# Performance work log

Measured on AMD Instinct MI355X. Metric: run time of the kernel, lower is better.

## Reference

```python
import jax, jax.numpy as jnp
import numpy as np

N_HEADS = 4
N_HIDDEN = 64  # out_features (concat=False)
MASK_FILL = -9e15
ADJ_THRESH = 0.05


def setup_inputs() -> dict:
    key = jax.random.key(0)
    k1, k2, k3, k4 = jax.random.split(key, 4)
    B, S, N, F = 32, 20, 128, 64
    h = jax.random.normal(k1, (B, S, N, F), dtype=jnp.float32)
    adj_mat = jax.random.uniform(k2, (B, S, N, N), dtype=jnp.float32)
    W = jax.random.normal(k3, (F, N_HEADS * N_HIDDEN), dtype=jnp.float32) * (1.0 / np.sqrt(F))
    a = jax.random.normal(k4, (N_HEADS, 2 * N_HIDDEN, 1), dtype=jnp.float32) * 0.1
    return {"h": h, "adj_mat": adj_mat, "W": W, "a": a}


def reference(h, adj_mat, W, a):
    B, S, N, _ = h.shape
    # Linear projection (no bias); dropout is a no-op (training=False)
    ht = jnp.einsum('bsnf,fo->bsno', h, W)
    # (B, S, H, N, D)
    ht = ht.reshape(B, S, N, N_HEADS, N_HIDDEN).transpose(0, 1, 3, 2, 4)
    a_src = a[:, :N_HIDDEN, 0]   # (H, D)
    a_tgt = a[:, N_HIDDEN:, 0]   # (H, D)
    src = jnp.einsum('bshnd,hd->bshn', ht, a_src)  # (B,S,H,N)
    tgt = jnp.einsum('bshnd,hd->bshn', ht, a_tgt)
    # additive sigmoid score: e_ij = sigmoid(src_i + tgt_j)
    e = jax.nn.sigmoid(src[..., :, None] + tgt[..., None, :])  # (B,S,H,N,N)
    mask = (adj_mat < ADJ_THRESH)[:, :, None, :, :]  # broadcast over heads
    e = jnp.where(mask, MASK_FILL, e)
    attn = jax.nn.softmax(e, axis=-1)
    h_prime = jnp.einsum('bshij,bshjd->bshid', attn, ht)
    # concat=False -> mean over heads
    return h_prime.mean(axis=2)  # (B,S,N,D)
```

## Files before the change

kernel.cpp:

```cpp
#include <hip/hip_runtime.h>
#include <hip/hip_bf16.h>

#define ADJ_TH 0.05f

typedef __bf16 bf16x8 __attribute__((ext_vector_type(8)));
typedef __bf16 bf16x4 __attribute__((ext_vector_type(4)));
typedef float  f32x4  __attribute__((ext_vector_type(4)));

__global__ __launch_bounds__(256)
void prep_kernel(const float* __restrict__ W, const float* __restrict__ a,
                 __bf16* __restrict__ Wt, __bf16* __restrict__ WAt) {
    const int t = threadIdx.x;
    if (blockIdx.x == 0) {
        #pragma unroll 4
        for (int r = 0; r < 64; ++r) {
            int id = r * 256 + t;
            Wt[(id & 255) * 64 + (id >> 8)] = (__bf16)W[id];
        }
    } else {
        for (int id = t; id < 1024; id += 256) {
            int n = id >> 6, f = id & 63;
            float s = 0.f;
            if (n < 8) {
                int hh = n >> 1, st = n & 1;
                #pragma unroll 8
                for (int d = 0; d < 64; ++d)
                    s += W[f * 256 + hh * 64 + d] * a[hh * 128 + st * 64 + d];
            }
            WAt[n * 64 + f] = (__bf16)s;
        }
    }
}

__device__ __forceinline__ int sw_idx(int o, int i) {
    return o * 128 + ((((i >> 3) ^ o) & 15) << 3) + (i & 7);
}

__global__ __launch_bounds__(256, 3)
void gat_main_kernel(const float* __restrict__ hg, const float* __restrict__ adj,
                     const __bf16* __restrict__ Wt, const __bf16* __restrict__ WAt,
                     float* __restrict__ out)
{
    const int bs  = blockIdx.x;
    const int tid = threadIdx.x;
    const int w   = tid >> 6;
    const int l   = tid & 63;
    const int l15 = l & 15;
    const int l4  = l >> 4;

    __shared__ __bf16   ht_t[128 * 128];
    __shared__ float    src_sh[4][128];
    __shared__ float    tgt_sh[4][128];
    __shared__ unsigned mask_sh[512];

    const float* hb = hg  + (size_t)bs * 8192;
    const float* ab = adj + (size_t)bs * 16384;

    #pragma unroll 8
    for (int it = 0; it < 64; ++it) {
        int row = 32 * w + (it >> 1);
        int col = ((it & 1) << 6) + l;
        unsigned long long bal = __ballot(ab[row * 128 + col] < ADJ_TH);
        if (l < 2) mask_sh[row * 4 + ((it & 1) << 1) + l] = (unsigned)(bal >> (32 * l));
    }

    bf16x8 af[2][2];
    #pragma unroll
    for (int m2 = 0; m2 < 2; ++m2) {
        int row = 16 * (2 * w + m2) + l15;
        #pragma unroll
        for (int ks = 0; ks < 2; ++ks) {
            const float4* p4 = reinterpret_cast<const float4*>(hb + row * 64 + 8 * l4 + 32 * ks);
            float4 lo = p4[0], hi = p4[1];
            bf16x8 v;
            v[0]=(__bf16)lo.x; v[1]=(__bf16)lo.y; v[2]=(__bf16)lo.z; v[3]=(__bf16)lo.w;
            v[4]=(__bf16)hi.x; v[5]=(__bf16)hi.y; v[6]=(__bf16)hi.z; v[7]=(__bf16)hi.w;
            af[m2][ks] = v;
        }
    }

    {
        bf16x8 wa0 = *reinterpret_cast<const bf16x8*>(WAt + l15 * 64 + 8 * l4);
        bf16x8 wa1 = *reinterpret_cast<const bf16x8*>(WAt + l15 * 64 + 8 * l4 + 32);
        #pragma unroll
        for (int m2 = 0; m2 < 2; ++m2) {
            f32x4 acc = {0.f,0.f,0.f,0.f};
            acc = __builtin_amdgcn_mfma_f32_16x16x32_bf16(af[m2][0], wa0, acc, 0,0,0);
            acc = __builtin_amdgcn_mfma_f32_16x16x32_bf16(af[m2][1], wa1, acc, 0,0,0);
            if (l15 < 8) {
                int hh = l15 >> 1;
                float* dst = (l15 & 1) ? tgt_sh[hh] : src_sh[hh];
                int i0 = 16 * (2 * w + m2) + 4 * l4;
                #pragma unroll
                for (int r = 0; r < 4; ++r) dst[i0 + r] = acc[r];
            }
        }
    }

    f32x4 acc2[2][4];
    #pragma unroll
    for (int m2 = 0; m2 < 2; ++m2)
        #pragma unroll
        for (int nt = 0; nt < 4; ++nt) { f32x4 z = {0.f,0.f,0.f,0.f}; acc2[m2][nt] = z; }

    #pragma unroll 1
    for (int p = 0; p < 2; ++p) {
        #pragma unroll
        for (int nt = 0; nt < 8; ++nt) {
            int oloc = 16 * nt + l15;
            const __bf16* wp = Wt + (size_t)(128 * p + oloc) * 64 + 8 * l4;
            bf16x8 b0 = *reinterpret_cast<const bf16x8*>(wp);
            bf16x8 b1 = *reinterpret_cast<const bf16x8*>(wp + 32);
            #pragma unroll
            for (int m2 = 0; m2 < 2; ++m2) {
                f32x4 acc = {0.f,0.f,0.f,0.f};
                acc = __builtin_amdgcn_mfma_f32_16x16x32_bf16(af[m2][0], b0, acc, 0,0,0);
                acc = __builtin_amdgcn_mfma_f32_16x16x32_bf16(af[m2][1], b1, acc, 0,0,0);
                int i0 = 16 * (2 * w + m2) + 4 * l4;
                bf16x4 st;
                st[0]=(__bf16)acc[0]; st[1]=(__bf16)acc[1];
                st[2]=(__bf16)acc[2]; st[3]=(__bf16)acc[3];
                *reinterpret_cast<bf16x4*>(&ht_t[sw_idx(oloc, i0)]) = st;
            }
        }
        __syncthreads();

        #pragma unroll 1
        for (int hp = 0; hp < 2; ++hp) {
            int hh = 2 * p + hp;
            bf16x8 pa[2][4];
            #pragma unroll
            for (int m2 = 0; m2 < 2; ++m2) {
                int irow = 16 * (2 * w + m2) + l15;
                float si = src_sh[hh][irow];
                uint4 mm = *reinterpret_cast<const uint4*>(&mask_sh[irow * 4]);
                unsigned mw[4] = {mm.x, mm.y, mm.z, mm.w};
                float pf[4][8];
                float dloc = 0.f;
                #pragma unroll
                for (int ks = 0; ks < 4; ++ks) {
                    const float4* tp = reinterpret_cast<const float4*>(&tgt_sh[hh][8 * l4 + 32 * ks]);
                    float4 t0 = tp[0], t1 = tp[1];
                    float tg[8] = {t0.x,t0.y,t0.z,t0.w,t1.x,t1.y,t1.z,t1.w};
                    #pragma unroll
                    for (int e = 0; e < 8; ++e) {
                        float x  = si + tg[e];
                        float sg = __builtin_amdgcn_rcpf(1.0f + __expf(-x));
                        float pe = __expf(sg);
                        float pv = ((mw[ks] >> (8 * l4 + e)) & 1u) ? 0.f : pe;
                        pf[ks][e] = pv;
                        dloc += pv;
                    }
                }
                dloc += __shfl_xor(dloc, 16);
                dloc += __shfl_xor(dloc, 32);
                float scale = 0.25f * __builtin_amdgcn_rcpf(fmaxf(dloc, 1e-20f));
                #pragma unroll
                for (int ks = 0; ks < 4; ++ks) {
                    bf16x8 v;
                    #pragma unroll
                    for (int e = 0; e < 8; ++e) v[e] = (__bf16)(pf[ks][e] * scale);
                    pa[m2][ks] = v;
                }
            }

            #pragma unroll
            for (int nt = 0; nt < 4; ++nt)
                #pragma unroll
                for (int ks = 0; ks < 4; ++ks) {
                    bf16x8 b = *reinterpret_cast<const bf16x8*>(
                        &ht_t[sw_idx(64 * hp + 16 * nt + l15, 8 * l4 + 32 * ks)]);
                    acc2[0][nt] = __builtin_amdgcn_mfma_f32_16x16x32_bf16(pa[0][ks], b, acc2[0][nt], 0,0,0);
                    acc2[1][nt] = __builtin_amdgcn_mfma_f32_16x16x32_bf16(pa[1][ks], b, acc2[1][nt], 0,0,0);
                }
        }
        __syncthreads();
    }

    float* ob = out + (size_t)bs * 8192;
    #pragma unroll
    for (int m2 = 0; m2 < 2; ++m2)
        #pragma unroll
        for (int nt = 0; nt < 4; ++nt)
            #pragma unroll
            for (int r = 0; r < 4; ++r)
                ob[(32 * w + 16 * m2 + 4 * l4 + r) * 64 + 16 * nt + l15] = acc2[m2][nt][r];
}

extern "C" void kernel_launch(void* const* d_in, const int* in_sizes, int n_in,
                              void* d_out, int out_size, void* d_ws, size_t ws_size,
                              hipStream_t stream) {
    const float* h   = (const float*)d_in[0];
    const float* adj = (const float*)d_in[1];
    const float* W   = (const float*)d_in[2];
    const float* a   = (const float*)d_in[3];
    float* out = (float*)d_out;

    __bf16* Wt  = (__bf16*)d_ws;
    __bf16* WAt = (__bf16*)((char*)d_ws + 32768);

    prep_kernel<<<2, 256, 0, stream>>>(W, a, Wt, WAt);
    gat_main_kernel<<<640, 256, 0, stream>>>(h, adj, Wt, WAt, out);
}
```

Baseline: 165.6 us.

## Parallelize prep kernel, vectorize adjacency mask loads, overlap with first projection

```diff
diff --git a/kernel.cpp b/kernel.cpp
--- a/kernel.cpp
+++ b/kernel.cpp
@@ -10,25 +10,25 @@
 __global__ __launch_bounds__(256)
 void prep_kernel(const float* __restrict__ W, const float* __restrict__ a,
                  __bf16* __restrict__ Wt, __bf16* __restrict__ WAt) {
-    const int t = threadIdx.x;
-    if (blockIdx.x == 0) {
-        #pragma unroll 4
-        for (int r = 0; r < 64; ++r) {
-            int id = r * 256 + t;
-            Wt[(id & 255) * 64 + (id >> 8)] = (__bf16)W[id];
-        }
+    const int t = threadIdx.x, blk = blockIdx.x;
+    if (blk < 64) {
+        int id = blk * 256 + t;
+        int o = id >> 6, k = id & 63;
+        Wt[o * 64 + k] = (__bf16)W[k * 256 + o];
+    } else if (blk < 72) {
+        int n = blk - 64, hh = n >> 1, st = n & 1;
+        int f = t >> 2, p = t & 3;
+        const float* wp = W + f * 256 + hh * 64 + p * 16;
+        const float* ap = a + hh * 128 + st * 64 + p * 16;
+        float s = 0.f;
+        #pragma unroll
+        for (int d = 0; d < 16; ++d) s += wp[d] * ap[d];
+        s += __shfl_xor(s, 1);
+        s += __shfl_xor(s, 2);
+        if (p == 0) WAt[n * 64 + f] = (__bf16)s;
     } else {
-        for (int id = t; id < 1024; id += 256) {
-            int n = id >> 6, f = id & 63;
-            float s = 0.f;
-            if (n < 8) {
-                int hh = n >> 1, st = n & 1;
-                #pragma unroll 8
-                for (int d = 0; d < 64; ++d)
-                    s += W[f * 256 + hh * 64 + d] * a[hh * 128 + st * 64 + d];
-            }
-            WAt[n * 64 + f] = (__bf16)s;
-        }
+        WAt[512 + t] = (__bf16)0.f;
+        WAt[768 + t] = (__bf16)0.f;
     }
 }
 
@@ -56,14 +56,6 @@
     const float* hb = hg  + (size_t)bs * 8192;
     const float* ab = adj + (size_t)bs * 16384;
 
-    #pragma unroll 8
-    for (int it = 0; it < 64; ++it) {
-        int row = 32 * w + (it >> 1);
-        int col = ((it & 1) << 6) + l;
-        unsigned long long bal = __ballot(ab[row * 128 + col] < ADJ_TH);
-        if (l < 2) mask_sh[row * 4 + ((it & 1) << 1) + l] = (unsigned)(bal >> (32 * l));
-    }
-
     bf16x8 af[2][2];
     #pragma unroll
     for (int m2 = 0; m2 < 2; ++m2) {
@@ -97,14 +89,7 @@
         }
     }
 
-    f32x4 acc2[2][4];
-    #pragma unroll
-    for (int m2 = 0; m2 < 2; ++m2)
-        #pragma unroll
-        for (int nt = 0; nt < 4; ++nt) { f32x4 z = {0.f,0.f,0.f,0.f}; acc2[m2][nt] = z; }
-
-    #pragma unroll 1
-    for (int p = 0; p < 2; ++p) {
+    auto gemm1 = [&](int p) {
         #pragma unroll
         for (int nt = 0; nt < 8; ++nt) {
             int oloc = 16 * nt + l15;
@@ -123,11 +108,47 @@
                 *reinterpret_cast<bf16x4*>(&ht_t[sw_idx(oloc, i0)]) = st;
             }
         }
-        __syncthreads();
-
+    };
+
+    gemm1(0);
+
+    #pragma unroll 4
+    for (int rd = 0; rd < 16; ++rd) {
+        float4 f = *reinterpret_cast<const float4*>(ab + rd * 1024 + w * 256 + 4 * l);
+        unsigned long long b0 = __ballot(f.x < ADJ_TH);
+        unsigned long long b1 = __ballot(f.y < ADJ_TH);
+        unsigned long long b2 = __ballot(f.z < ADJ_TH);
+        unsigned long long b3 = __ballot(f.w < ADJ_TH);
+        if (l < 2) {
+            int row = 8 * rd + 2 * w + l;
+            uint4 v;
+            v.x = (unsigned)(b0 >> (32 * l));
+            v.y = (unsigned)(b1 >> (32 * l));
+            v.z = (unsigned)(b2 >> (32 * l));
+            v.w = (unsigned)(b3 >> (32 * l));
+            *reinterpret_cast<uint4*>(&mask_sh[row * 4]) = v;
+        }
+    }
+
+    f32x4 acc2[2][4];
+    #pragma unroll
+    for (int m2 = 0; m2 < 2; ++m2)
+        #pragma unroll
+        for (int nt = 0; nt < 4; ++nt) { f32x4 z = {0.f,0.f,0.f,0.f}; acc2[m2][nt] = z; }
+
+    auto phase2 = [&](int p) {
         #pragma unroll 1
         for (int hp = 0; hp < 2; ++hp) {
             int hh = 2 * p + hp;
+            float tg[4][8];
+            #pragma unroll
+            for (int ks = 0; ks < 4; ++ks) {
+                const float4* tp = reinterpret_cast<const float4*>(&tgt_sh[hh][8 * l4 + 32 * ks]);
+                float4 t0 = tp[0], t1 = tp[1];
+                tg[ks][0]=t0.x; tg[ks][1]=t0.y; tg[ks][2]=t0.z; tg[ks][3]=t0.w;
+                tg[ks][4]=t1.x; tg[ks][5]=t1.y; tg[ks][6]=t1.z; tg[ks][7]=t1.w;
+            }
+
             bf16x8 pa[2][4];
             #pragma unroll
             for (int m2 = 0; m2 < 2; ++m2) {
@@ -139,15 +160,12 @@
                 float dloc = 0.f;
                 #pragma unroll
                 for (int ks = 0; ks < 4; ++ks) {
-                    const float4* tp = reinterpret_cast<const float4*>(&tgt_sh[hh][8 * l4 + 32 * ks]);
-                    float4 t0 = tp[0], t1 = tp[1];
-                    float tg[8] = {t0.x,t0.y,t0.z,t0.w,t1.x,t1.y,t1.z,t1.w};
                     #pragma unroll
                     for (int e = 0; e < 8; ++e) {
-                        float x  = si + tg[e];
+                        float x  = si + tg[ks][e];
                         float sg = __builtin_amdgcn_rcpf(1.0f + __expf(-x));
                         float pe = __expf(sg);
-                        float pv = ((mw[ks] >> (8 * l4 + e)) & 1u) ? 0.f : pe;
+                        float pv = ((mw[e & 3] >> (8 * ks + 2 * l4 + (e >> 2))) & 1u) ? 0.f : pe;
                         pf[ks][e] = pv;
                         dloc += pv;
                     }
@@ -174,8 +192,14 @@
                     acc2[1][nt] = __builtin_amdgcn_mfma_f32_16x16x32_bf16(pa[1][ks], b, acc2[1][nt], 0,0,0);
                 }
         }
-        __syncthreads();
-    }
+    };
+
+    __syncthreads();
+    phase2(0);
+    __syncthreads();
+    gemm1(1);
+    __syncthreads();
+    phase2(1);
 
     float* ob = out + (size_t)bs * 8192;
     #pragma unroll
@@ -199,6 +223,6 @@
     __bf16* Wt  = (__bf16*)d_ws;
     __bf16* WAt = (__bf16*)((char*)d_ws + 32768);
 
-    prep_kernel<<<2, 256, 0, stream>>>(W, a, Wt, WAt);
+    prep_kernel<<<73, 256, 0, stream>>>(W, a, Wt, WAt);
     gat_main_kernel<<<640, 256, 0, stream>>>(h, adj, Wt, WAt, out);
 }
```

Measured after the change: 138.3 us. 1.2x faster.
